# Optimization experiments

Measured on AMD Instinct MI355X. Metric: run time of the kernel, lower is better.

Reference implementation:

```python
import jax, jax.numpy as jnp
import numpy as np


def _patch_points(P):
    # replicates: meshgrid(y,x,z, indexing='ij'); points = cat([zz, yy, xx], -1).reshape(-1,3)
    lin = jnp.linspace(-1.0, 1.0, P)
    a, b, c = jnp.meshgrid(lin, lin, lin, indexing='ij')  # all identical linspaces
    pts = jnp.stack([c, b, a], axis=-1).reshape(-1, 3)     # (P^3, 3)
    return pts


def _proj_locations(points, angles):
    # Tomographic projection geometry (generate_projections_location):
    # rotate points about the detector-vertical axis and keep in-plane coords.
    # points: (N,3); angles: (A,) radians. Returns (A, N, 2) grid coords (x, y)
    # in grid_sample convention (last dim: x indexes width, y indexes height).
    p0 = points[:, 0]
    p1 = points[:, 1]
    p2 = points[:, 2]
    c = jnp.cos(angles)[:, None]   # (A,1)
    s = jnp.sin(angles)[:, None]
    gx = p0[None, :] * c + p2[None, :] * s          # (A, N)
    gy = jnp.broadcast_to(p1[None, :], gx.shape)    # (A, N)
    return jnp.stack([gx, gy], axis=-1)             # (A, N, 2)


def _bilinear_sample(img, grid):
    # img: (C,H,W); grid: (N,2) in [-1,1], align_corners=True, padding zeros.
    C, H, W = img.shape
    ix = (grid[:, 0] + 1.0) * 0.5 * (W - 1)
    iy = (grid[:, 1] + 1.0) * 0.5 * (H - 1)
    ix0 = jnp.floor(ix)
    iy0 = jnp.floor(iy)
    ix1 = ix0 + 1.0
    iy1 = iy0 + 1.0
    wx1 = ix - ix0
    wx0 = 1.0 - wx1
    wy1 = iy - iy0
    wy0 = 1.0 - wy1

    def corner(iyc, ixc, w):
        valid = (ixc >= 0) & (ixc <= W - 1) & (iyc >= 0) & (iyc <= H - 1)
        xi = jnp.clip(ixc, 0, W - 1).astype(jnp.int32)
        yi = jnp.clip(iyc, 0, H - 1).astype(jnp.int32)
        return img[:, yi, xi] * (w * valid)[None, :]   # (C,N)

    return (corner(iy0, ix0, wy0 * wx0) + corner(iy0, ix1, wy0 * wx1)
            + corner(iy1, ix0, wy1 * wx0) + corner(iy1, ix1, wy1 * wx1))


def setup_inputs() -> dict:
    key = jax.random.key(0)
    k1, k2 = jax.random.split(key)
    B, A, P = 128, 121, 33
    x = jax.random.normal(k1, (B, A, P, P), dtype=jnp.float32)
    angles = jax.random.uniform(k2, (1, A), dtype=jnp.float32,
                                minval=0.0, maxval=2.0 * np.pi)
    return {"x": x, "angles": angles}


def reference(x, angles):
    B, A, P, _ = x.shape
    pts = _patch_points(P)                       # (P^3, 3)
    grids = _proj_locations(pts, angles[0])      # (A, P^3, 2)
    xs = jnp.transpose(x, (1, 0, 2, 3))          # (A, B, P, P)

    def body(acc, inp):
        xi, gi = inp                             # (B,P,P), (P^3,2)
        return acc + _bilinear_sample(xi, gi), None

    acc0 = jnp.zeros((B, P * P * P), dtype=x.dtype)
    acc, _ = jax.lax.scan(body, acc0, (xs, grids))
    x_fbp = acc.reshape(B, P, P, P) / A
    return x_fbp
```

## Files before the change

### kernel.cpp

```cpp
#include <hip/hip_runtime.h>
#include <hip/hip_fp16.h>
#include <math.h>


#define PDIM 33
#define PP   1089
#define A_   121
#define K_   3993
#define KP   4032
#define MP   1152
#define MT2  18
#define NT2  66
#define NWG  1188
#define OUTB 35937

typedef _Float16 f16x8 __attribute__((ext_vector_type(8)));
typedef float    f32x4 __attribute__((ext_vector_type(4)));

typedef __attribute__((address_space(1))) const unsigned int* gp_t;
typedef __attribute__((address_space(3))) unsigned int*       lp_t;


__global__ __launch_bounds__(256)
void prep_kernel(const float* __restrict__ x, const float* __restrict__ angles,
                 __half* __restrict__ Xt, __half* __restrict__ W)
{
    const int blk = blockIdx.x;
    const int t   = threadIdx.x;

    if (blk < PDIM * 128) {
        const int n  = blk;
        const int i1 = n >> 7;
        const int b  = n & 127;
        const float* src = x + (size_t)b * (A_ * PP) + (size_t)i1 * PDIM;
        unsigned int* dst = (unsigned int*)(Xt + (size_t)n * KP);
        for (int e = t; e < KP / 2; e += 256) {
            int kk0 = 2 * e, kk1 = 2 * e + 1;
            float v0 = 0.0f, v1 = 0.0f;
            if (kk0 < K_) {
                int j = kk0 / PDIM, k = kk0 - j * PDIM;
                v0 = src[(size_t)j * PP + k];
            }
            if (kk1 < K_) {
                int j = kk1 / PDIM, k = kk1 - j * PDIM;
                v1 = src[(size_t)j * PP + k];
            }
            dst[e] = __builtin_bit_cast(unsigned int,
                         __builtin_amdgcn_cvt_pkrtz(v0, v1));
        }
    } else {
        const int n = blk - PDIM * 128;
        __half* row = W + (size_t)n * KP;
        int4 zz = make_int4(0, 0, 0, 0);
        for (int e = t; e < KP / 8; e += 256)
            ((int4*)row)[e] = zz;
        __syncthreads();
        if (n >= PP || t >= A_) return;
        const int j  = t;
        const int i0 = n / PDIM;
        const int i2 = n - i0 * PDIM;
        float s, c;
        sincosf(angles[j], &s, &c);
        float ix = fmaf((float)(i2 - 16), c, fmaf((float)(i0 - 16), s, 16.0f));
        float fl = floorf(ix);
        int   k0 = (int)fl;
        float w1 = ix - fl;
        float w0 = 1.0f - w1;
        __half* seg = row + j * PDIM;
        if (k0 >= 0     && k0 < PDIM)     seg[k0]     = __float2half_rn(w0);
        if (k0 + 1 >= 0 && k0 + 1 < PDIM) seg[k0 + 1] = __float2half_rn(w1);
    }
}

__global__ __launch_bounds__(256)
void gemm_kernel(const __half* __restrict__ W, const __half* __restrict__ Xt,
                 float* __restrict__ out, float invA)
{
    __shared__ _Float16 As[64 * 64];
    __shared__ _Float16 Bs[64 * 64];

    const int b0  = blockIdx.x;
    const int xcd = b0 & 7;
    const int pos = b0 >> 3;
    const int d   = (xcd < 4) ? xcd * 149 + pos
                              : 596 + (xcd - 4) * 148 + pos;
    int tileM, tileN;
    if (d < 324) {
        int c = d / 162, l = d - c * 162;
        tileM = l / 9;
        tileN = c * 9 + (l - tileM * 9);
    } else {
        int dd = d - 324;
        int c = dd / 144, l = dd - c * 144;
        tileM = l >> 3;
        tileN = 18 + c * 8 + (l & 7);
    }

    const int t     = threadIdx.x;
    const int lane  = t & 63;
    const int wave  = t >> 6;
    const int warpM = wave >> 1;
    const int warpN = wave & 1;
    const int quad  = lane >> 4;
    const int l15   = lane & 15;

    f32x4 acc[2][2] = {};

    const __half* Ab = W  + (size_t)(tileM * 64) * KP;
    const __half* Bb = Xt + (size_t)(tileN * 64) * KP;

    int srow[2], ssego[2];
#pragma unroll
    for (int i = 0; i < 2; ++i) {
        int cidx = t + i * 256;
        int row  = cidx >> 3;
        int seg  = cidx & 7;
        srow[i]  = row;
        ssego[i] = (seg ^ (row & 7)) * 8;
    }

    int arow[2], brow[2];
#pragma unroll
    for (int s = 0; s < 2; ++s) {
        arow[s] = warpM * 32 + s * 16 + l15;
        brow[s] = warpN * 32 + s * 16 + l15;
    }

    for (int kb = 0; kb < KP; kb += 64) {
        __syncthreads();
#pragma unroll
        for (int i = 0; i < 2; ++i) {
            const __half* ga = Ab + (size_t)srow[i] * KP + kb + ssego[i];
            const __half* gb = Bb + (size_t)srow[i] * KP + kb + ssego[i];
            __builtin_amdgcn_global_load_lds((gp_t)(const void*)ga,
                (lp_t)(void*)&As[(t + i * 256) * 8], 16, 0, 0);
            __builtin_amdgcn_global_load_lds((gp_t)(const void*)gb,
                (lp_t)(void*)&Bs[(t + i * 256) * 8], 16, 0, 0);
        }
        __syncthreads();

        f16x8 af[2][2], bf[2][2];
#pragma unroll
        for (int h = 0; h < 2; ++h) {
#pragma unroll
            for (int s = 0; s < 2; ++s) {
                int ks = h * 4 + quad;
                af[h][s] = *(const f16x8*)&As[arow[s] * 64 + ((ks ^ (arow[s] & 7)) * 8)];
                bf[h][s] = *(const f16x8*)&Bs[brow[s] * 64 + ((ks ^ (brow[s] & 7)) * 8)];
            }
        }
#pragma unroll
        for (int h = 0; h < 2; ++h)
#pragma unroll
            for (int ms = 0; ms < 2; ++ms)
#pragma unroll
                for (int ns = 0; ns < 2; ++ns)
                    acc[ms][ns] = __builtin_amdgcn_mfma_f32_16x16x32_f16(
                        af[h][ms], bf[h][ns], acc[ms][ns], 0, 0, 0);
    }

#pragma unroll
    for (int ns = 0; ns < 2; ++ns) {
        int nglob = tileN * 64 + warpN * 32 + ns * 16 + l15;
        int i1 = nglob >> 7;
        int b  = nglob & 127;
        float* ob = out + (size_t)b * OUTB + (size_t)i1 * PDIM;
#pragma unroll
        for (int ms = 0; ms < 2; ++ms) {
#pragma unroll
            for (int r = 0; r < 4; ++r) {
                int m = tileM * 64 + warpM * 32 + ms * 16 + quad * 4 + r;
                if (m < PP) {
                    int i0 = m / PDIM;
                    int i2 = m - i0 * PDIM;
                    ob[(size_t)i0 * PP + i2] = acc[ms][ns][r] * invA;
                }
            }
        }
    }
}


#define ROWW 47
#define PADL 7
#define BLK  384
#define NV   3
#define GRID 1280

typedef _Float16 h2v __attribute__((ext_vector_type(2)));

#if defined(__has_builtin)
#if __has_builtin(__builtin_amdgcn_fractf)
#define FRACTF(x) __builtin_amdgcn_fractf(x)
#endif
#endif
#ifndef FRACTF
#define FRACTF(x) ((x) - floorf(x))
#endif

__device__ __forceinline__ float fdot2u(unsigned int a, unsigned int b, float c)
{
    return __builtin_amdgcn_fdot2(__builtin_bit_cast(h2v, a),
                                  __builtin_bit_cast(h2v, b), c, false);
}

__global__ __launch_bounds__(BLK)
void fbp_adjoint_kernel(const float* __restrict__ x,
                        const float* __restrict__ angles,
                        float* __restrict__ out,
                        int nslice, float invA)
{
    __shared__ unsigned int dr[A_ * ROWW];
    __shared__ float2       cs_lds[A_];

    const int t = threadIdx.x;
    for (int j = t; j < A_; j += BLK) {
        float s, c;
        sincosf(angles[j], &s, &c);
        cs_lds[j] = make_float2(c, s);
    }

    float u0[NV], u2[NV];
#pragma unroll
    for (int nn = 0; nn < NV; ++nn) {
        int n  = t + nn * BLK;
        int nc = (n < PP) ? n : (PP - 1);
        int q0 = nc / PDIM;
        int q2 = nc - q0 * PDIM;
        u0[nn] = (float)(q0 - 16);
        u2[nn] = (float)(q2 - 16);
    }

    for (int slice = blockIdx.x; slice < nslice; slice += GRID) {
        if (slice != (int)blockIdx.x) __syncthreads();
        const int hb = slice / PDIM;
        const int i1 = slice - hb * PDIM;
        const int b0 = 2 * hb;
        const float* r0 = x + (size_t)b0 * (A_ * PP) + (size_t)i1 * PDIM;
        const float* r1 = r0 + (size_t)(A_ * PP);
        for (int e = t; e < A_ * ROWW; e += BLK) {
            int j = e / ROWW;
            int p = e - j * ROWW;
            int k = p - PADL;
            float f0 = 0.0f, f1 = 0.0f;
            if (k >= 0 && k < PDIM) {
                size_t o = (size_t)j * PP + k;
                f0 = r0[o];
                f1 = r1[o];
            }
            dr[e] = __builtin_bit_cast(unsigned int,
                        __halves2half2(__float2half_rn(f0), __float2half_rn(f1)));
        }
        __syncthreads();

        float a0[NV] = {0.0f, 0.0f, 0.0f};
        float a1[NV] = {0.0f, 0.0f, 0.0f};
#pragma unroll 2
        for (int j = 0; j < A_; ++j) {
            float2 cj = cs_lds[j];
            const unsigned int* base = &dr[j * ROWW];
#pragma unroll
            for (int nn = 0; nn < NV; ++nn) {
                float ixp = fmaf(u2[nn], cj.x, fmaf(u0[nn], cj.y, 23.0f));
                int   kp  = (int)ixp;
                float w1  = FRACTF(ixp);
                unsigned int wp = __builtin_bit_cast(unsigned int,
                                    __builtin_amdgcn_cvt_pkrtz(1.0f - w1, w1));
                unsigned int d0 = base[kp];
                unsigned int d1 = base[kp + 1];
                unsigned int p0 = __builtin_amdgcn_perm(d1, d0, 0x05040100u);
                unsigned int p1 = __builtin_amdgcn_perm(d1, d0, 0x07060302u);
                a0[nn] = fdot2u(p0, wp, a0[nn]);
                a1[nn] = fdot2u(p1, wp, a1[nn]);
            }
        }

        float* ob0 = out + (size_t)b0 * OUTB + (size_t)i1 * PDIM;
        float* ob1 = ob0 + (size_t)OUTB;
#pragma unroll
        for (int nn = 0; nn < NV; ++nn) {
            int n = t + nn * BLK;
            if (n < PP) {
                int q0 = n / PDIM;
                int q2 = n - q0 * PDIM;
                size_t o = (size_t)q0 * PP + q2;
                ob0[o] = a0[nn] * invA;
                ob1[o] = a1[nn] * invA;
            }
        }
    }
}


extern "C" void kernel_launch(void* const* d_in, const int* in_sizes, int n_in,
                              void* d_out, int out_size, void* d_ws, size_t ws_size,
                              hipStream_t stream)
{
    const float* x      = (const float*)d_in[0];
    const float* angles = (const float*)d_in[1];
    float* out          = (float*)d_out;

    const int A = in_sizes[1];
    const int B = in_sizes[0] / (A * PP);
    const float invA = 1.0f / (float)A;

    const size_t wBytes  = (size_t)MP * KP * sizeof(__half);
    const size_t xtBytes = (size_t)(PDIM * B) * KP * sizeof(__half);

    if (ws_size >= wBytes + xtBytes && A == A_ && B == 128) {
        __half* W  = (__half*)d_ws;
        __half* Xt = (__half*)((char*)d_ws + wBytes);
        prep_kernel<<<PDIM * B + MP, 256, 0, stream>>>(x, angles, Xt, W);
        gemm_kernel<<<NWG, 256, 0, stream>>>(W, Xt, out, invA);
    } else {
        const int nslice = (B / 2) * PDIM;
        dim3 grid(GRID < nslice ? GRID : nslice);
        fbp_adjoint_kernel<<<grid, BLK, 0, stream>>>(x, angles, out,
                                                     nslice, invA);
    }
}
```

Before: 178.2 us.

## Generate interpolation weights inside GEMM and stage transpose through LDS

The dense sparse-weight matrix W is no longer precomputed in global memory. Each GEMM block now computes the bilinear weights for its A tile on the fly from per-block sincos values and writes them into LDS. This removes the W zero-fill and write and the matching global loads of A tiles. The prep kernel is also restructured to read x with coalesced float4 loads into LDS before writing the transposed fp16 Xt rows. In exchange the GEMM inner loop gains ALU work and branchy selects for weight generation.

```diff
diff --git a/kernel.cpp b/kernel.cpp
--- a/kernel.cpp
+++ b/kernel.cpp
@@ -8,89 +8,113 @@
 #define A_   121
 #define K_   3993
 #define KP   4032
-#define MP   1152
 #define MT2  18
 #define NT2  66
 #define NWG  1188
 #define OUTB 35937
+#define XTB  2048
 
 typedef _Float16 f16x8 __attribute__((ext_vector_type(8)));
 typedef float    f32x4 __attribute__((ext_vector_type(4)));
+typedef _Float16 h2v   __attribute__((ext_vector_type(2)));
 
 typedef __attribute__((address_space(1))) const unsigned int* gp_t;
 typedef __attribute__((address_space(3))) unsigned int*       lp_t;
 
+static __device__ __forceinline__ unsigned short cvt1_rtz(float v)
+{
+    return (unsigned short)__builtin_bit_cast(unsigned int,
+               __builtin_amdgcn_cvt_pkrtz(v, v));
+}
+
 
 __global__ __launch_bounds__(256)
-void prep_kernel(const float* __restrict__ x, const float* __restrict__ angles,
-                 __half* __restrict__ Xt, __half* __restrict__ W)
-{
+void prep_kernel(const float* __restrict__ x, __half* __restrict__ Xt)
+{
+    __shared__ unsigned short lh[8752];
     const int blk = blockIdx.x;
     const int t   = threadIdx.x;
-
-    if (blk < PDIM * 128) {
-        const int n  = blk;
-        const int i1 = n >> 7;
-        const int b  = n & 127;
-        const float* src = x + (size_t)b * (A_ * PP) + (size_t)i1 * PDIM;
-        unsigned int* dst = (unsigned int*)(Xt + (size_t)n * KP);
-        for (int e = t; e < KP / 2; e += 256) {
-            int kk0 = 2 * e, kk1 = 2 * e + 1;
-            float v0 = 0.0f, v1 = 0.0f;
-            if (kk0 < K_) {
-                int j = kk0 / PDIM, k = kk0 - j * PDIM;
-                v0 = src[(size_t)j * PP + k];
-            }
-            if (kk1 < K_) {
-                int j = kk1 / PDIM, k = kk1 - j * PDIM;
-                v1 = src[(size_t)j * PP + k];
-            }
-            dst[e] = __builtin_bit_cast(unsigned int,
-                         __builtin_amdgcn_cvt_pkrtz(v0, v1));
-        }
+    const int b   = blk >> 4;
+    const int g   = blk & 15;
+
+    const float* src = x + (size_t)b * (A_ * PP)
+                         + (size_t)(g < 15 ? g * 8712 : 120 * PP);
+    const int nTot = (g < 15) ? 8712 : PP;
+
+    {
+        const int sh = ((16 - (int)((size_t)src & 15)) >> 2) & 3;
+        if (t < sh) lh[t] = cvt1_rtz(src[t]);
+        const int nv = (nTot - sh) >> 2;
+        const float4* s4 = (const float4*)(src + sh);
+        for (int e = t; e < nv; e += 256) {
+            float4 v = s4[e];
+            int o = sh + 4 * e;
+            lh[o + 0] = cvt1_rtz(v.x);
+            lh[o + 1] = cvt1_rtz(v.y);
+            lh[o + 2] = cvt1_rtz(v.z);
+            lh[o + 3] = cvt1_rtz(v.w);
+        }
+        const int tb  = sh + 4 * nv;
+        const int rem = nTot - tb;
+        if (t < rem) lh[tb + t] = cvt1_rtz(src[tb + t]);
+    }
+    __syncthreads();
+
+    if (g < 15) {
+#define LH8(c) (unsigned int)(((c) < rem8) ? lh[j0p * PP + ib + k0p + (c)] \
+                                           : lh[(j0p + 1) * PP + ib + ((c) - rem8)])
+        for (int e = t; e < 33 * 33; e += 256) {
+            int i1 = e / 33, q = e - i1 * 33;
+            int le = 8 * q;
+            int j0p = le / 33;
+            int k0p = le - j0p * 33;
+            int rem8 = 33 - k0p;
+            int ib = i1 * PDIM;
+            unsigned int d0 = LH8(0) | (LH8(1) << 16);
+            unsigned int d1 = LH8(2) | (LH8(3) << 16);
+            unsigned int d2 = LH8(4) | (LH8(5) << 16);
+            unsigned int d3 = LH8(6) | (LH8(7) << 16);
+            uint4* drow = (uint4*)(Xt + (size_t)(i1 * 128 + b) * KP + g * 264);
+            drow[q] = make_uint4(d0, d1, d2, d3);
+        }
+#undef LH8
     } else {
-        const int n = blk - PDIM * 128;
-        __half* row = W + (size_t)n * KP;
-        int4 zz = make_int4(0, 0, 0, 0);
-        for (int e = t; e < KP / 8; e += 256)
-            ((int4*)row)[e] = zz;
-        __syncthreads();
-        if (n >= PP || t >= A_) return;
-        const int j  = t;
-        const int i0 = n / PDIM;
-        const int i2 = n - i0 * PDIM;
-        float s, c;
-        sincosf(angles[j], &s, &c);
-        float ix = fmaf((float)(i2 - 16), c, fmaf((float)(i0 - 16), s, 16.0f));
-        float fl = floorf(ix);
-        int   k0 = (int)fl;
-        float w1 = ix - fl;
-        float w0 = 1.0f - w1;
-        __half* seg = row + j * PDIM;
-        if (k0 >= 0     && k0 < PDIM)     seg[k0]     = __float2half_rn(w0);
-        if (k0 + 1 >= 0 && k0 + 1 < PDIM) seg[k0 + 1] = __float2half_rn(w1);
+#define LHT(c) (unsigned int)((le + (c) < PDIM) ? lh[ib + le + (c)] : 0u)
+        for (int e = t; e < 33 * 9; e += 256) {
+            int i1 = e / 9, q = e - i1 * 9;
+            int le = 8 * q;
+            int ib = i1 * PDIM;
+            unsigned int d0 = LHT(0) | (LHT(1) << 16);
+            unsigned int d1 = LHT(2) | (LHT(3) << 16);
+            unsigned int d2 = LHT(4) | (LHT(5) << 16);
+            unsigned int d3 = LHT(6) | (LHT(7) << 16);
+            uint4* drow = (uint4*)(Xt + (size_t)(i1 * 128 + b) * KP + 3960);
+            drow[q] = make_uint4(d0, d1, d2, d3);
+        }
+#undef LHT
     }
 }
 
 __global__ __launch_bounds__(256)
-void gemm_kernel(const __half* __restrict__ W, const __half* __restrict__ Xt,
+void gemm_kernel(const __half* __restrict__ Xt, const float* __restrict__ angles,
                  float* __restrict__ out, float invA)
 {
     __shared__ _Float16 As[64 * 64];
     __shared__ _Float16 Bs[64 * 64];
+    __shared__ float2   csl[A_];
 
     const int b0  = blockIdx.x;
     const int xcd = b0 & 7;
     const int pos = b0 >> 3;
-    const int d   = (xcd < 4) ? xcd * 149 + pos
+    const int dd0 = (xcd < 4) ? xcd * 149 + pos
                               : 596 + (xcd - 4) * 148 + pos;
     int tileM, tileN;
-    if (d < 324) {
-        int c = d / 162, l = d - c * 162;
+    if (dd0 < 324) {
+        int c = dd0 / 162, l = dd0 - c * 162;
         tileM = l / 9;
         tileN = c * 9 + (l - tileM * 9);
     } else {
-        int dd = d - 324;
+        int dd = dd0 - 324;
         int c = dd / 144, l = dd - c * 144;
         tileM = l >> 3;
         tileN = 18 + c * 8 + (l & 7);
@@ -104,9 +128,14 @@
     const int quad  = lane >> 4;
     const int l15   = lane & 15;
 
+    if (t < A_) {
+        float s, c;
+        sincosf(angles[t], &s, &c);
+        csl[t] = make_float2(c, s);
+    }
+
     f32x4 acc[2][2] = {};
 
-    const __half* Ab = W  + (size_t)(tileM * 64) * KP;
     const __half* Bb = Xt + (size_t)(tileN * 64) * KP;
 
     int srow[2], ssego[2];
@@ -119,6 +148,18 @@
         ssego[i] = (seg ^ (row & 7)) * 8;
     }
 
+    const int r   = t & 63;
+    const int q16 = t >> 6;
+    const int m   = tileM * 64 + r;
+    const bool mv = (m < PP);
+    const int i0m = m / PDIM;
+    const int i2m = m - i0m * PDIM;
+    const float u0 = (float)(i0m - 16);
+    const float u2 = (float)(i2m - 16);
+    unsigned int* As32 = (unsigned int*)As;
+    const int wa0 = r * 32 + (((2 * q16)     ^ (r & 7)) * 4);
+    const int wa1 = r * 32 + (((2 * q16 + 1) ^ (r & 7)) * 4);
+
     int arow[2], brow[2];
 #pragma unroll
     for (int s = 0; s < 2; ++s) {
@@ -130,12 +171,56 @@
         __syncthreads();
 #pragma unroll
         for (int i = 0; i < 2; ++i) {
-            const __half* ga = Ab + (size_t)srow[i] * KP + kb + ssego[i];
             const __half* gb = Bb + (size_t)srow[i] * KP + kb + ssego[i];
-            __builtin_amdgcn_global_load_lds((gp_t)(const void*)ga,
-                (lp_t)(void*)&As[(t + i * 256) * 8], 16, 0, 0);
             __builtin_amdgcn_global_load_lds((gp_t)(const void*)gb,
                 (lp_t)(void*)&Bs[(t + i * 256) * 8], 16, 0, 0);
+        }
+        {
+            const int kkb  = kb + q16 * 16;
+            const int ja   = kkb / PDIM;
+            const int jb   = ja + 1;
+            const int jb33 = jb * PDIM;
+            const int ka   = kkb - ja * PDIM;
+            int k0a = -100, k0b = -100;
+            unsigned int w0ah = 0, w1ah = 0, w0bh = 0, w1bh = 0;
+            if (mv && ja < A_) {
+                float2 cs = csl[ja];
+                float ix = fmaf(u2, cs.x, fmaf(u0, cs.y, 16.0f));
+                float fl = floorf(ix);
+                k0a = (int)fl;
+                float w1 = ix - fl;
+                w0ah = (unsigned int)__builtin_bit_cast(unsigned short,
+                           __float2half_rn(1.0f - w1));
+                w1ah = (unsigned int)__builtin_bit_cast(unsigned short,
+                           __float2half_rn(w1));
+            }
+            if (mv && jb < A_) {
+                float2 cs = csl[jb];
+                float ix = fmaf(u2, cs.x, fmaf(u0, cs.y, 16.0f));
+                float fl = floorf(ix);
+                k0b = (int)fl;
+                float w1 = ix - fl;
+                w0bh = (unsigned int)__builtin_bit_cast(unsigned short,
+                           __float2half_rn(1.0f - w1));
+                w1bh = (unsigned int)__builtin_bit_cast(unsigned short,
+                           __float2half_rn(w1));
+            }
+#define HS(k, k0v, w0v, w1v) \
+    ((k) == (k0v) ? (w0v) : ((k) == (k0v) + 1 ? (w1v) : 0u))
+#define HV(kc) ((kkb + (kc)) < jb33 ? HS(ka + (kc), k0a, w0ah, w1ah) \
+                                    : HS((kkb + (kc)) - jb33, k0b, w0bh, w1bh))
+            unsigned int d0 = HV(0)  | (HV(1)  << 16);
+            unsigned int d1 = HV(2)  | (HV(3)  << 16);
+            unsigned int d2 = HV(4)  | (HV(5)  << 16);
+            unsigned int d3 = HV(6)  | (HV(7)  << 16);
+            unsigned int d4 = HV(8)  | (HV(9)  << 16);
+            unsigned int d5 = HV(10) | (HV(11) << 16);
+            unsigned int d6 = HV(12) | (HV(13) << 16);
+            unsigned int d7 = HV(14) | (HV(15) << 16);
+#undef HV
+#undef HS
+            *(uint4*)(As32 + wa0) = make_uint4(d0, d1, d2, d3);
+            *(uint4*)(As32 + wa1) = make_uint4(d4, d5, d6, d7);
         }
         __syncthreads();
 
@@ -168,12 +253,12 @@
 #pragma unroll
         for (int ms = 0; ms < 2; ++ms) {
 #pragma unroll
-            for (int r = 0; r < 4; ++r) {
-                int m = tileM * 64 + warpM * 32 + ms * 16 + quad * 4 + r;
-                if (m < PP) {
-                    int i0 = m / PDIM;
-                    int i2 = m - i0 * PDIM;
-                    ob[(size_t)i0 * PP + i2] = acc[ms][ns][r] * invA;
+            for (int rr = 0; rr < 4; ++rr) {
+                int mm = tileM * 64 + warpM * 32 + ms * 16 + quad * 4 + rr;
+                if (mm < PP) {
+                    int i0 = mm / PDIM;
+                    int i2 = mm - i0 * PDIM;
+                    ob[(size_t)i0 * PP + i2] = acc[ms][ns][rr] * invA;
                 }
             }
         }
@@ -186,8 +271,6 @@
 #define BLK  384
 #define NV   3
 #define GRID 1280
-
-typedef _Float16 h2v __attribute__((ext_vector_type(2)));
 
 #if defined(__has_builtin)
 #if __has_builtin(__builtin_amdgcn_fractf)
@@ -304,14 +387,12 @@
     const int B = in_sizes[0] / (A * PP);
     const float invA = 1.0f / (float)A;
 
-    const size_t wBytes  = (size_t)MP * KP * sizeof(__half);
     const size_t xtBytes = (size_t)(PDIM * B) * KP * sizeof(__half);
 
-    if (ws_size >= wBytes + xtBytes && A == A_ && B == 128) {
-        __half* W  = (__half*)d_ws;
-        __half* Xt = (__half*)((char*)d_ws + wBytes);
-        prep_kernel<<<PDIM * B + MP, 256, 0, stream>>>(x, angles, Xt, W);
-        gemm_kernel<<<NWG, 256, 0, stream>>>(W, Xt, out, invA);
+    if (ws_size >= xtBytes && A == A_ && B == 128) {
+        __half* Xt = (__half*)d_ws;
+        prep_kernel<<<XTB, 256, 0, stream>>>(x, Xt);
+        gemm_kernel<<<NWG, 256, 0, stream>>>(Xt, angles, out, invA);
     } else {
         const int nslice = (B / 2) * PDIM;
         dim3 grid(GRID < nslice ? GRID : nslice);
```

Measured after the change: 259.7 us. 1.46x slower.

## Fuse prep and GEMM into one persistent kernel with per-tile readiness flags

Applied to the files above, without the earlier changes.

Merges the prep kernel, which converts x to fp16 Xt and builds the sparse interpolation weight matrix W, into the GEMM kernel. Blocks claim prep chunks through a global atomic work counter, tally completed chunks per 64-row group, and then each GEMM tile spin-waits only until its own A and B row groups are ready. This removes the kernel boundary and lets GEMM tiles start while other prep work is still running. It adds a memset launch, atomics and spin-waits, and relies on all blocks being co-resident to avoid deadlock.

```diff
diff --git a/kernel.cpp b/kernel.cpp
--- a/kernel.cpp
+++ b/kernel.cpp
@@ -13,71 +13,95 @@
 #define NT2  66
 #define NWG  1188
 #define OUTB 35937
+#define NXCH 4224
+#define NCHUNK (NXCH + MP)
+#define NGRP 84
 
 typedef _Float16 f16x8 __attribute__((ext_vector_type(8)));
 typedef float    f32x4 __attribute__((ext_vector_type(4)));
+typedef _Float16 h2v   __attribute__((ext_vector_type(2)));
 
 typedef __attribute__((address_space(1))) const unsigned int* gp_t;
 typedef __attribute__((address_space(3))) unsigned int*       lp_t;
 
 
 __global__ __launch_bounds__(256)
-void prep_kernel(const float* __restrict__ x, const float* __restrict__ angles,
-                 __half* __restrict__ Xt, __half* __restrict__ W)
-{
-    const int blk = blockIdx.x;
-    const int t   = threadIdx.x;
-
-    if (blk < PDIM * 128) {
-        const int n  = blk;
-        const int i1 = n >> 7;
-        const int b  = n & 127;
-        const float* src = x + (size_t)b * (A_ * PP) + (size_t)i1 * PDIM;
-        unsigned int* dst = (unsigned int*)(Xt + (size_t)n * KP);
-        for (int e = t; e < KP / 2; e += 256) {
-            int kk0 = 2 * e, kk1 = 2 * e + 1;
-            float v0 = 0.0f, v1 = 0.0f;
-            if (kk0 < K_) {
-                int j = kk0 / PDIM, k = kk0 - j * PDIM;
-                v0 = src[(size_t)j * PP + k];
-            }
-            if (kk1 < K_) {
-                int j = kk1 / PDIM, k = kk1 - j * PDIM;
-                v1 = src[(size_t)j * PP + k];
-            }
-            dst[e] = __builtin_bit_cast(unsigned int,
-                         __builtin_amdgcn_cvt_pkrtz(v0, v1));
-        }
-    } else {
-        const int n = blk - PDIM * 128;
-        __half* row = W + (size_t)n * KP;
-        int4 zz = make_int4(0, 0, 0, 0);
-        for (int e = t; e < KP / 8; e += 256)
-            ((int4*)row)[e] = zz;
-        __syncthreads();
-        if (n >= PP || t >= A_) return;
-        const int j  = t;
-        const int i0 = n / PDIM;
-        const int i2 = n - i0 * PDIM;
-        float s, c;
-        sincosf(angles[j], &s, &c);
-        float ix = fmaf((float)(i2 - 16), c, fmaf((float)(i0 - 16), s, 16.0f));
-        float fl = floorf(ix);
-        int   k0 = (int)fl;
-        float w1 = ix - fl;
-        float w0 = 1.0f - w1;
-        __half* seg = row + j * PDIM;
-        if (k0 >= 0     && k0 < PDIM)     seg[k0]     = __float2half_rn(w0);
-        if (k0 + 1 >= 0 && k0 + 1 < PDIM) seg[k0 + 1] = __float2half_rn(w1);
-    }
-}
-
-__global__ __launch_bounds__(256)
-void gemm_kernel(const __half* __restrict__ W, const __half* __restrict__ Xt,
-                 float* __restrict__ out, float invA)
+void fused_kernel(const float* __restrict__ x, const float* __restrict__ angles,
+                  __half* __restrict__ W, __half* __restrict__ Xt,
+                  int* __restrict__ flags, float* __restrict__ out, float invA)
 {
     __shared__ _Float16 As[64 * 64];
     __shared__ _Float16 Bs[64 * 64];
+    __shared__ int chunk_s;
+    __shared__ int lcnt[NGRP];
+
+    int* nextp = flags;
+    int* cnt   = flags + 1;
+
+    const int t = threadIdx.x;
+    for (int g = t; g < NGRP; g += 256) lcnt[g] = 0;
+
+    for (;;) {
+        __syncthreads();
+        if (t == 0) chunk_s = atomicAdd(nextp, 1);
+        __syncthreads();
+        const int c = chunk_s;
+        if (c >= NCHUNK) break;
+
+        if (c < NXCH) {
+            const int n  = c;
+            const int i1 = n >> 7;
+            const int b  = n & 127;
+            const float* src = x + (size_t)b * (A_ * PP) + (size_t)i1 * PDIM;
+            unsigned int* dst = (unsigned int*)(Xt + (size_t)n * KP);
+            for (int e = t; e < KP / 2; e += 256) {
+                int kk0 = 2 * e, kk1 = 2 * e + 1;
+                float v0 = 0.0f, v1 = 0.0f;
+                if (kk0 < K_) {
+                    int j = kk0 / PDIM, k = kk0 - j * PDIM;
+                    v0 = src[(size_t)j * PP + k];
+                }
+                if (kk1 < K_) {
+                    int j = kk1 / PDIM, k = kk1 - j * PDIM;
+                    v1 = src[(size_t)j * PP + k];
+                }
+                dst[e] = __builtin_bit_cast(unsigned int,
+                             __builtin_amdgcn_cvt_pkrtz(v0, v1));
+            }
+        } else {
+            const int n = c - NXCH;
+            __half* row = W + (size_t)n * KP;
+            int4 zz = make_int4(0, 0, 0, 0);
+            for (int e = t; e < KP / 8; e += 256)
+                ((int4*)row)[e] = zz;
+            __syncthreads();
+            if (n < PP && t < A_) {
+                const int j  = t;
+                const int i0 = n / PDIM;
+                const int i2 = n - i0 * PDIM;
+                float s, cc;
+                sincosf(angles[j], &s, &cc);
+                float ix = fmaf((float)(i2 - 16), cc,
+                                fmaf((float)(i0 - 16), s, 16.0f));
+                float fl = floorf(ix);
+                int   k0 = (int)fl;
+                float w1 = ix - fl;
+                float w0 = 1.0f - w1;
+                __half* seg = row + j * PDIM;
+                if (k0 >= 0     && k0 < PDIM)     seg[k0]     = __float2half_rn(w0);
+                if (k0 + 1 >= 0 && k0 + 1 < PDIM) seg[k0 + 1] = __float2half_rn(w1);
+            }
+        }
+        if (t == 0)
+            ++lcnt[c < NXCH ? (c >> 6) : 66 + ((c - NXCH) >> 6)];
+    }
+
+    __syncthreads();
+    if (t == 0) {
+        __threadfence();
+        for (int g = 0; g < NGRP; ++g)
+            if (lcnt[g]) atomicAdd(&cnt[g], lcnt[g]);
+    }
 
     const int b0  = blockIdx.x;
     const int xcd = b0 & 7;
@@ -96,7 +120,17 @@
         tileN = 18 + c * 8 + (l & 7);
     }
 
-    const int t     = threadIdx.x;
+    if (t == 0) {
+        while (__hip_atomic_load(&cnt[66 + tileM], __ATOMIC_ACQUIRE,
+                                 __HIP_MEMORY_SCOPE_AGENT) < 64)
+            __builtin_amdgcn_s_sleep(2);
+        while (__hip_atomic_load(&cnt[tileN], __ATOMIC_ACQUIRE,
+                                 __HIP_MEMORY_SCOPE_AGENT) < 64)
+            __builtin_amdgcn_s_sleep(2);
+        __threadfence();
+    }
+    __syncthreads();
+
     const int lane  = t & 63;
     const int wave  = t >> 6;
     const int warpM = wave >> 1;
@@ -186,8 +220,6 @@
 #define BLK  384
 #define NV   3
 #define GRID 1280
-
-typedef _Float16 h2v __attribute__((ext_vector_type(2)));
 
 #if defined(__has_builtin)
 #if __has_builtin(__builtin_amdgcn_fractf)
@@ -306,12 +338,15 @@
 
     const size_t wBytes  = (size_t)MP * KP * sizeof(__half);
     const size_t xtBytes = (size_t)(PDIM * B) * KP * sizeof(__half);
-
-    if (ws_size >= wBytes + xtBytes && A == A_ && B == 128) {
+    const size_t fBytes  = (size_t)(1 + NGRP) * sizeof(int);
+
+    if (ws_size >= wBytes + xtBytes + fBytes && A == A_ && B == 128) {
         __half* W  = (__half*)d_ws;
         __half* Xt = (__half*)((char*)d_ws + wBytes);
-        prep_kernel<<<PDIM * B + MP, 256, 0, stream>>>(x, angles, Xt, W);
-        gemm_kernel<<<NWG, 256, 0, stream>>>(W, Xt, out, invA);
+        int* flags = (int*)((char*)d_ws + wBytes + xtBytes);
+        hipMemsetAsync(flags, 0, fBytes, stream);
+        fused_kernel<<<NWG, 256, 0, stream>>>(x, angles, W, Xt, flags,
+                                              out, invA);
     } else {
         const int nslice = (B / 2) * PDIM;
         dim3 grid(GRID < nslice ? GRID : nslice);
```

After: 383.9 us. +115.4%, slower.
